# Kernel tuning notes

Measured on AMD Instinct MI355X. Metric: run time of the kernel, lower is better.

## Reference

```python
import jax, jax.numpy as jnp
import numpy as np


def setup_inputs() -> dict:
    key = jax.random.key(0)
    kq, kk, kv = jax.random.split(key, 3)
    B, H, N, D = 4, 8, 2048, 64
    q = jax.random.normal(kq, (B, H, N, D), dtype=jnp.float32)
    k = jax.random.normal(kk, (B, H, N, D), dtype=jnp.float32)
    v = jax.random.normal(kv, (B, H, N, D), dtype=jnp.float32)
    return {"q": q, "k": k, "v": v}


def reference(q, k, v):
    # Naive attention exactly as the torch module: full [B,H,N,N] scores.
    scale = q.shape[-1] ** -0.5
    sim = jnp.einsum('bhid,bhjd->bhij', q, k) * scale  # [B,H,N,N]
    attn = jax.nn.softmax(sim, axis=-1)
    # dropout p=0.0 -> identity (module default; eval mode)
    out = jnp.einsum('bhij,bhjd->bhid', attn, v)  # [B,H,N,D]
    return out
```

## Files before the change

### kernel.cpp

```cpp
#include <hip/hip_runtime.h>

#define NN   2048
#define DD   64
#define KVB  64
#define NTW  16
#define BH   32
#define BHND (BH * NN * DD)
#define SC   0.18033688f
#define TSH  8192

typedef float    f32x4  __attribute__((ext_vector_type(4)));
typedef short    bf16x8 __attribute__((ext_vector_type(8)));
typedef unsigned u32x4  __attribute__((ext_vector_type(4)));

#define WAIT_VM0()   asm volatile("s_waitcnt vmcnt(0)" ::: "memory")
#define SFENCE()     __builtin_amdgcn_sched_barrier(0)
#define SBAR()       __builtin_amdgcn_s_barrier()

__device__ __forceinline__ short f2bf(float x){
    unsigned u = __float_as_uint(x);
    u += 0x7FFF + ((u >> 16) & 1);
    return (short)(u >> 16);
}

__device__ __forceinline__ unsigned cvt_pk(float lo, float hi){
    unsigned r;
    asm("v_cvt_pk_bf16_f32 %0, %1, %2" : "=v"(r) : "v"(lo), "v"(hi));
    return r;
}

__device__ __forceinline__ float exp2_fast(float x){
    float r;
    asm("v_exp_f32 %0, %1" : "=v"(r) : "v"(x));
    return r;
}

__device__ __forceinline__ void gload_lds16(const short* g, short* l) {
    __builtin_amdgcn_global_load_lds(
        (const __attribute__((address_space(1))) void*)g,
        (__attribute__((address_space(3))) void*)l, 16, 0, 0);
}

__global__ __launch_bounds__(256)
void prep_frag(const float* __restrict__ k, const float* __restrict__ v,
               short* __restrict__ fr)
{
    const int tile = blockIdx.x;
    const int bh   = blockIdx.y;
    const int tid  = threadIdx.x;
    const int lane = tid & 63;
    const int f    = tid >> 6;
    const int l16  = lane & 15;
    const int lg   = lane >> 4;
    const long base = (long)bh * NN * DD;
    const int  kv0  = tile * KVB;
    short* tb = fr + ((long)bh * 32 + tile) * TSH;

    {
        const float* src = k + base + (long)(kv0 + f * 16 + l16) * DD + lg * 8;
        #pragma unroll
        for (int c = 0; c < 2; ++c) {
            f32x4 x0 = *(const f32x4*)(src + c * 32);
            f32x4 x1 = *(const f32x4*)(src + c * 32 + 4);
            bf16x8 o;
            #pragma unroll
            for (int j = 0; j < 4; ++j) { o[j] = f2bf(x0[j]); o[4 + j] = f2bf(x1[j]); }
            *(bf16x8*)(tb + ((f * 2 + c) * 64 + lane) * 8) = o;
        }
    }
    {
        const float* vb = v + base;
        #pragma unroll
        for (int kk = 0; kk < 2; ++kk) {
            bf16x8 o;
            #pragma unroll
            for (int i = 0; i < 8; ++i) {
                float x = vb[(long)(kv0 + kk * 32 + (i >> 2) * 16 + lg * 4 + (i & 3)) * DD
                             + f * 16 + l16];
                o[i] = f2bf(x);
            }
            *(bf16x8*)(tb + ((8 + f * 2 + kk) * 64 + lane) * 8) = o;
        }
    }
}

__global__ __launch_bounds__(256, 2)
void attn_fwd_v21(const float* __restrict__ q,
                  const short* __restrict__ fr,
                  float* __restrict__ out)
{
    const int l     = blockIdx.x;
    const int xcd   = l & 7;
    const int idx   = l >> 3;
    const int qtile = idx & 15;
    const int bh    = xcd + 8 * (idx >> 4);

    const int tid   = threadIdx.x;
    const int wave  = tid >> 6;
    const int qg    = wave & 1;
    const int kvh   = wave >> 1;
    const int lane  = tid & 63;
    const int l16   = lane & 15;
    const int lg    = lane >> 4;

    __shared__ __align__(16) short lds_s[2][2][TSH];

    const long base  = (long)bh * NN * DD;
    const int  qrow0 = qtile * 128 + qg * 64;

    bf16x8 aq[4][2];
    #pragma unroll
    for (int j = 0; j < 4; ++j) {
        const float* qp = q + base + (long)(qrow0 + j * 16 + l16) * DD + lg * 8;
        #pragma unroll
        for (int c = 0; c < 2; ++c) {
            f32x4 x0 = *(const f32x4*)(qp + c * 32);
            f32x4 x1 = *(const f32x4*)(qp + c * 32 + 4);
            u32x4 pk;
            pk[0] = cvt_pk(x0[0] * SC, x0[1] * SC);
            pk[1] = cvt_pk(x0[2] * SC, x0[3] * SC);
            pk[2] = cvt_pk(x1[0] * SC, x1[1] * SC);
            pk[3] = cvt_pk(x1[2] * SC, x1[3] * SC);
            aq[j][c] = __builtin_bit_cast(bf16x8, pk);
        }
    }

    bf16x8 ones;
    #pragma unroll
    for (int ii = 0; ii < 8; ++ii) ones[ii] = (short)0x3F80;

    const short* fbase = fr + ((long)bh * 32 + kvh * NTW) * TSH + lane * 8;

    auto stage = [&](int buf, int tt) {
        const short* src = fbase + (long)tt * TSH + qg * 8 * 512;
        short* dst = &lds_s[kvh][buf][qg * 8 * 512];
        #pragma unroll
        for (int j = 0; j < 8; ++j)
            gload_lds16(src + j * 512, dst + j * 512);
    };

    f32x4 acc[4][4];
    f32x4 accS[4];
    #pragma unroll
    for (int t = 0; t < 4; ++t)
        #pragma unroll
        for (int j = 0; j < 4; ++j) acc[t][j] = f32x4{0.f, 0.f, 0.f, 0.f};
    #pragma unroll
    for (int j = 0; j < 4; ++j) accS[j] = f32x4{0.f, 0.f, 0.f, 0.f};

    stage(0, 0);

    for (int t = 0; t < NTW; ++t) {
        WAIT_VM0(); SFENCE();
        SBAR(); SFENCE();
        if (t + 1 < NTW) stage((t + 1) & 1, t + 1);

        const short* lb = &lds_s[kvh][t & 1][lane * 8];

        bf16x8 pa[4][2];
        #pragma unroll
        for (int h = 0; h < 2; ++h) {
            bf16x8 ka[2][2], bv[4];
            #pragma unroll
            for (int cb = 0; cb < 2; ++cb)
                #pragma unroll
                for (int c = 0; c < 2; ++c)
                    ka[cb][c] = *(const bf16x8*)(lb + (((2 * h + cb) * 2 + c)) * 512);
            #pragma unroll
            for (int t2 = 0; t2 < 4; ++t2)
                bv[t2] = *(const bf16x8*)(lb + (8 + t2 * 2 + h) * 512);

            f32x4 s[2][4];
            __builtin_amdgcn_s_setprio(1);
            #pragma unroll
            for (int cb = 0; cb < 2; ++cb)
                #pragma unroll
                for (int j = 0; j < 4; ++j) {
                    f32x4 z = f32x4{0.f, 0.f, 0.f, 0.f};
                    z = __builtin_amdgcn_mfma_f32_16x16x32_bf16(ka[cb][0], aq[j][0], z, 0, 0, 0);
                    z = __builtin_amdgcn_mfma_f32_16x16x32_bf16(ka[cb][1], aq[j][1], z, 0, 0, 0);
                    s[cb][j] = z;
                }
            __builtin_amdgcn_s_setprio(0);

            #pragma unroll
            for (int j = 0; j < 4; ++j) {
                #pragma unroll
                for (int cb = 0; cb < 2; ++cb)
                    #pragma unroll
                    for (int r = 0; r < 4; ++r)
                        s[cb][j][r] = exp2_fast(s[cb][j][r]);
                u32x4 w;
                w[0] = cvt_pk(s[0][j][0], s[0][j][1]);
                w[1] = cvt_pk(s[0][j][2], s[0][j][3]);
                w[2] = cvt_pk(s[1][j][0], s[1][j][1]);
                w[3] = cvt_pk(s[1][j][2], s[1][j][3]);
                pa[j][h] = __builtin_bit_cast(bf16x8, w);
            }

            __builtin_amdgcn_s_setprio(1);
            #pragma unroll
            for (int t2 = 0; t2 < 4; ++t2)
                #pragma unroll
                for (int j = 0; j < 4; ++j)
                    acc[t2][j] = __builtin_amdgcn_mfma_f32_16x16x32_bf16(pa[j][h], bv[t2], acc[t2][j], 0, 0, 0);
            #pragma unroll
            for (int j = 0; j < 4; ++j)
                accS[j] = __builtin_amdgcn_mfma_f32_16x16x32_bf16(pa[j][h], ones, accS[j], 0, 0, 0);
            __builtin_amdgcn_s_setprio(0);
        }
    }

    __syncthreads();

    float* slot = (float*)&lds_s[0][0][0];
    if (kvh == 1) {
        float* sp = slot + qg * 5120;
        #pragma unroll
        for (int t2 = 0; t2 < 4; ++t2)
            #pragma unroll
            for (int j = 0; j < 4; ++j)
                *(f32x4*)&sp[((t2 * 4 + j) * 64 + lane) * 4] = acc[t2][j];
        #pragma unroll
        for (int j = 0; j < 4; ++j)
            *(f32x4*)&sp[((16 + j) * 64 + lane) * 4] = accS[j];
    }
    __syncthreads();

    if (kvh == 0) {
        const float* sp = slot + qg * 5120;
        #pragma unroll
        for (int j = 0; j < 4; ++j)
            accS[j] += *(const f32x4*)&sp[((16 + j) * 64 + lane) * 4];
        float* op = out + base + (long)qrow0 * DD;
        #pragma unroll
        for (int j = 0; j < 4; ++j) {
            f32x4 inv;
            #pragma unroll
            for (int r = 0; r < 4; ++r) inv[r] = 1.f / accS[j][r];
            #pragma unroll
            for (int t2 = 0; t2 < 4; ++t2) {
                f32x4 o = acc[t2][j] + *(const f32x4*)&sp[((t2 * 4 + j) * 64 + lane) * 4];
                #pragma unroll
                for (int r = 0; r < 4; ++r)
                    op[(long)(j * 16 + lg * 4 + r) * DD + t2 * 16 + l16] = o[r] * inv[r];
            }
        }
    }
}

extern "C" void kernel_launch(void* const* d_in, const int* in_sizes, int n_in,
                              void* d_out, int out_size, void* d_ws, size_t ws_size,
                              hipStream_t stream) {
    const float* q = (const float*)d_in[0];
    const float* k = (const float*)d_in[1];
    const float* v = (const float*)d_in[2];
    float* out = (float*)d_out;

    short* fr = (short*)d_ws;
    prep_frag<<<dim3(32, BH), 256, 0, stream>>>(k, v, fr);
    attn_fwd_v21<<<512, 256, 0, stream>>>(q, fr, out);
    (void)ws_size;
}
```

Before: 52.12 us.

## Stage only K through LDS, load V fragments directly from global

The main loop now stages only K fragments into LDS, two KV tiles per iteration. V fragments are loaded straight from global memory into registers at the point of use. The aim is to halve LDS traffic and the number of barrier steps, trading that for exposed global-load latency on V inside the compute loop. The existing vmcnt(0) wait may also end up serialising on those V loads.

```diff
diff --git a/kernel.cpp b/kernel.cpp
--- a/kernel.cpp
+++ b/kernel.cpp
@@ -2,8 +2,7 @@
 
 #define NN   2048
 #define DD   64
-#define KVB  64
-#define NTW  16
+#define NTW  8
 #define BH   32
 #define BHND (BH * NN * DD)
 #define SC   0.18033688f
@@ -53,7 +52,7 @@
     const int l16  = lane & 15;
     const int lg   = lane >> 4;
     const long base = (long)bh * NN * DD;
-    const int  kv0  = tile * KVB;
+    const int  kv0  = tile * 64;
     short* tb = fr + ((long)bh * 32 + tile) * TSH;
 
     {
@@ -85,7 +84,7 @@
 }
 
 __global__ __launch_bounds__(256, 2)
-void attn_fwd_v21(const float* __restrict__ q,
+void attn_fwd_v25(const float* __restrict__ q,
                   const short* __restrict__ fr,
                   float* __restrict__ out)
 {
@@ -103,7 +102,7 @@
     const int l16   = lane & 15;
     const int lg    = lane >> 4;
 
-    __shared__ __align__(16) short lds_s[2][2][TSH];
+    __shared__ __align__(16) short k_lds[2][2][8192];
 
     const long base  = (long)bh * NN * DD;
     const int  qrow0 = qtile * 128 + qg * 64;
@@ -129,14 +128,17 @@
     #pragma unroll
     for (int ii = 0; ii < 8; ++ii) ones[ii] = (short)0x3F80;
 
-    const short* fbase = fr + ((long)bh * 32 + kvh * NTW) * TSH + lane * 8;
-
-    auto stage = [&](int buf, int tt) {
-        const short* src = fbase + (long)tt * TSH + qg * 8 * 512;
-        short* dst = &lds_s[kvh][buf][qg * 8 * 512];
-        #pragma unroll
-        for (int j = 0; j < 8; ++j)
-            gload_lds16(src + j * 512, dst + j * 512);
+    const short* fbase = fr + ((long)bh * 32 + kvh * 16) * TSH + lane * 8;
+
+    auto stageK = [&](int buf, int tt) {
+        const short* s0 = fbase + (long)(2 * tt) * TSH + qg * 4 * 512;
+        const short* s1 = fbase + (long)(2 * tt + 1) * TSH + qg * 4 * 512;
+        short* d0 = &k_lds[kvh][buf][qg * 4 * 512];
+        short* d1 = &k_lds[kvh][buf][4096 + qg * 4 * 512];
+        #pragma unroll
+        for (int j = 0; j < 4; ++j) gload_lds16(s0 + j * 512, d0 + j * 512);
+        #pragma unroll
+        for (int j = 0; j < 4; ++j) gload_lds16(s1 + j * 512, d1 + j * 512);
     };
 
     f32x4 acc[4][4];
@@ -148,72 +150,79 @@
     #pragma unroll
     for (int j = 0; j < 4; ++j) accS[j] = f32x4{0.f, 0.f, 0.f, 0.f};
 
-    stage(0, 0);
-
+    stageK(0, 0);
+
+    #pragma unroll 1
     for (int t = 0; t < NTW; ++t) {
         WAIT_VM0(); SFENCE();
         SBAR(); SFENCE();
-        if (t + 1 < NTW) stage((t + 1) & 1, t + 1);
-
-        const short* lb = &lds_s[kvh][t & 1][lane * 8];
-
-        bf16x8 pa[4][2];
-        #pragma unroll
-        for (int h = 0; h < 2; ++h) {
-            bf16x8 ka[2][2], bv[4];
-            #pragma unroll
-            for (int cb = 0; cb < 2; ++cb)
-                #pragma unroll
-                for (int c = 0; c < 2; ++c)
-                    ka[cb][c] = *(const bf16x8*)(lb + (((2 * h + cb) * 2 + c)) * 512);
-            #pragma unroll
-            for (int t2 = 0; t2 < 4; ++t2)
-                bv[t2] = *(const bf16x8*)(lb + (8 + t2 * 2 + h) * 512);
-
-            f32x4 s[2][4];
-            __builtin_amdgcn_s_setprio(1);
-            #pragma unroll
-            for (int cb = 0; cb < 2; ++cb)
+        if (t + 1 < NTW) stageK((t + 1) & 1, t + 1);
+
+        #pragma unroll
+        for (int u = 0; u < 2; ++u) {
+            const short* lb   = &k_lds[kvh][t & 1][u * 4096 + lane * 8];
+            const short* vsrc = fbase + (long)(2 * t + u) * TSH;
+
+            #pragma unroll
+            for (int kk = 0; kk < 2; ++kk) {
+                bf16x8 bvv[4];
+                #pragma unroll
+                for (int t2 = 0; t2 < 4; ++t2)
+                    bvv[t2] = *(const bf16x8*)(vsrc + (8 + t2 * 2 + kk) * 512);
+
+                bf16x8 ka[2][2];
+                #pragma unroll
+                for (int cb = 0; cb < 2; ++cb)
+                    #pragma unroll
+                    for (int c = 0; c < 2; ++c)
+                        ka[cb][c] = *(const bf16x8*)(lb + (((2 * kk + cb) * 2 + c)) * 512);
+
+                f32x4 s[2][4];
+                __builtin_amdgcn_s_setprio(1);
+                #pragma unroll
+                for (int cb = 0; cb < 2; ++cb)
+                    #pragma unroll
+                    for (int j = 0; j < 4; ++j) {
+                        f32x4 z = f32x4{0.f, 0.f, 0.f, 0.f};
+                        z = __builtin_amdgcn_mfma_f32_16x16x32_bf16(ka[cb][0], aq[j][0], z, 0, 0, 0);
+                        z = __builtin_amdgcn_mfma_f32_16x16x32_bf16(ka[cb][1], aq[j][1], z, 0, 0, 0);
+                        s[cb][j] = z;
+                    }
+                __builtin_amdgcn_s_setprio(0);
+
+                bf16x8 pa[4];
                 #pragma unroll
                 for (int j = 0; j < 4; ++j) {
-                    f32x4 z = f32x4{0.f, 0.f, 0.f, 0.f};
-                    z = __builtin_amdgcn_mfma_f32_16x16x32_bf16(ka[cb][0], aq[j][0], z, 0, 0, 0);
-                    z = __builtin_amdgcn_mfma_f32_16x16x32_bf16(ka[cb][1], aq[j][1], z, 0, 0, 0);
-                    s[cb][j] = z;
+                    #pragma unroll
+                    for (int cb = 0; cb < 2; ++cb)
+                        #pragma unroll
+                        for (int r = 0; r < 4; ++r)
+                            s[cb][j][r] = exp2_fast(s[cb][j][r]);
+                    u32x4 w;
+                    w[0] = cvt_pk(s[0][j][0], s[0][j][1]);
+                    w[1] = cvt_pk(s[0][j][2], s[0][j][3]);
+                    w[2] = cvt_pk(s[1][j][0], s[1][j][1]);
+                    w[3] = cvt_pk(s[1][j][2], s[1][j][3]);
+                    pa[j] = __builtin_bit_cast(bf16x8, w);
                 }
-            __builtin_amdgcn_s_setprio(0);
-
-            #pragma unroll
-            for (int j = 0; j < 4; ++j) {
-                #pragma unroll
-                for (int cb = 0; cb < 2; ++cb)
-                    #pragma unroll
-                    for (int r = 0; r < 4; ++r)
-                        s[cb][j][r] = exp2_fast(s[cb][j][r]);
-                u32x4 w;
-                w[0] = cvt_pk(s[0][j][0], s[0][j][1]);
-                w[1] = cvt_pk(s[0][j][2], s[0][j][3]);
-                w[2] = cvt_pk(s[1][j][0], s[1][j][1]);
-                w[3] = cvt_pk(s[1][j][2], s[1][j][3]);
-                pa[j][h] = __builtin_bit_cast(bf16x8, w);
+
+                __builtin_amdgcn_s_setprio(1);
+                #pragma unroll
+                for (int t2 = 0; t2 < 4; ++t2)
+                    #pragma unroll
+                    for (int j = 0; j < 4; ++j)
+                        acc[t2][j] = __builtin_amdgcn_mfma_f32_16x16x32_bf16(pa[j], bvv[t2], acc[t2][j], 0, 0, 0);
+                #pragma unroll
+                for (int j = 0; j < 4; ++j)
+                    accS[j] = __builtin_amdgcn_mfma_f32_16x16x32_bf16(pa[j], ones, accS[j], 0, 0, 0);
+                __builtin_amdgcn_s_setprio(0);
             }
-
-            __builtin_amdgcn_s_setprio(1);
-            #pragma unroll
-            for (int t2 = 0; t2 < 4; ++t2)
-                #pragma unroll
-                for (int j = 0; j < 4; ++j)
-                    acc[t2][j] = __builtin_amdgcn_mfma_f32_16x16x32_bf16(pa[j][h], bv[t2], acc[t2][j], 0, 0, 0);
-            #pragma unroll
-            for (int j = 0; j < 4; ++j)
-                accS[j] = __builtin_amdgcn_mfma_f32_16x16x32_bf16(pa[j][h], ones, accS[j], 0, 0, 0);
-            __builtin_amdgcn_s_setprio(0);
         }
     }
 
     __syncthreads();
 
-    float* slot = (float*)&lds_s[0][0][0];
+    float* slot = (float*)&k_lds[0][0][0];
     if (kvh == 1) {
         float* sp = slot + qg * 5120;
         #pragma unroll
@@ -259,6 +268,6 @@
 
     short* fr = (short*)d_ws;
     prep_frag<<<dim3(32, BH), 256, 0, stream>>>(k, v, fr);
-    attn_fwd_v21<<<512, 256, 0, stream>>>(q, fr, out);
+    attn_fwd_v25<<<512, 256, 0, stream>>>(q, fr, out);
     (void)ws_size;
 }
```

Result: no change. 51.77 us (-0.7%).
